# Kernel optimization log

Hardware: AMD Instinct MI355X
Metric: run time of the kernel (lower is better)

## Reference

```python
import jax, jax.numpy as jnp
import numpy as np

T = 0.07
TOPK = 5

def _l2norm(x, axis=-1, eps=1e-12):
    n = jnp.sqrt(jnp.sum(x * x, axis=axis, keepdims=True))
    return x / jnp.maximum(n, eps)

def setup_inputs() -> dict:
    key = jax.random.key(0)
    k1, k2, k3, k4, k5 = jax.random.split(key, 5)
    b, nc, dim, dim_mlp, K = 256, 5, 128, 2048, 65536
    q = jax.random.normal(k1, (b, nc, dim), jnp.float32)
    k = jax.random.normal(k2, (b, dim), jnp.float32)
    q_backbone = jax.random.normal(k3, (b, nc, dim_mlp), jnp.float32)
    # queues are column-normalized buffers, as in __init__
    queue = _l2norm(jax.random.normal(k4, (dim, K), jnp.float32), axis=0)
    queue_backbone = _l2norm(jax.random.normal(k5, (dim_mlp, K), jnp.float32), axis=0)
    return {"q": q, "k": k, "q_backbone": q_backbone,
            "queue": queue, "queue_backbone": queue_backbone}

def reference(q, k, q_backbone, queue, queue_backbone):
    b, nc, dim = q.shape
    dim_mlp = q_backbone.shape[-1]
    qn = _l2norm(q)                 # [b, nc, dim]
    kn = _l2norm(k)                 # [b, dim]
    qb = _l2norm(q_backbone)        # [b, nc, dim_mlp]

    # positive logits: each crop vs its key
    l_pos = jnp.einsum('bnd,bd->bn', qn, kn).reshape(-1, 1)      # [b*nc, 1]
    # negative logits vs queue
    l_neg = jnp.einsum('nc,ck->nk', qn.reshape(-1, dim), queue)  # [b*nc, K]
    logits = jnp.concatenate([l_pos, l_neg], axis=1) / T
    labels = jnp.zeros((logits.shape[0],), dtype=jnp.int32)

    # backbone-space similarities to pick top-k neighbors
    l_neg_backbone = jnp.einsum('nc,ck->nk', qb.reshape(-1, dim_mlp), queue_backbone)

    # pull_topk: softmax CE pulling toward top-k backbone neighbors.
    # scatter-mask + masked mean == gather log-softmax at top-k indices (indices distinct)
    _, knn_idx = jax.lax.top_k(l_neg_backbone, TOPK)             # [b*nc, TOPK]
    log_prob = jax.nn.log_softmax(l_neg / T, axis=1)             # [b*nc, K]
    pos_logp = jnp.take_along_axis(log_prob, knn_idx, axis=1)    # [b*nc, TOPK]
    loss = -jnp.mean(jnp.mean(pos_logp, axis=1))
    return logits, labels, loss
```

## Files before the change

kernel.cpp:

```cpp
#include <hip/hip_runtime.h>
#include <hip/hip_bf16.h>

#define M_     1280
#define DIM    128
#define DMLP   2048
#define KQ     65536
#define NCOLS  65537ull
#define NTOPK  5
#define NCHUNK 256
#define NBLK1  512
#define NTK    32
#define INV_T  14.285714285714286f

typedef __attribute__((ext_vector_type(8))) short bf16x8;
typedef __attribute__((ext_vector_type(4))) float f32x4;

static __device__ __forceinline__ unsigned short f2bf(float x){
  union { __hip_bfloat16 h; unsigned short u; } cv;
  cv.h = __float2bfloat16(x);
  return cv.u;
}

#define GLDS16(gp, lp) __builtin_amdgcn_global_load_lds( \
    (const __attribute__((address_space(1))) void*)(gp), \
    (__attribute__((address_space(3))) void*)(lp), 16, 0, 0)

#define BAR()   asm volatile("s_barrier" ::: "memory")
#define VMW(n)  asm volatile("s_waitcnt vmcnt(" #n ")" ::: "memory")

__global__ __launch_bounds__(256) void transpose_bf16(
    const float* __restrict__ in, unsigned short* __restrict__ out, int R, int C){
  __shared__ float tile[64][65];
  const int c0 = blockIdx.x * 64, r0 = blockIdx.y * 64;
  const int t = threadIdx.x;
  #pragma unroll
  for (int i = 0; i < 4; ++i){
    int lin = t + i * 256;
    int rr = lin >> 4;
    int cc = (lin & 15) * 4;
    const float4 v = *(const float4*)(in + (size_t)(r0 + rr) * C + c0 + cc);
    tile[rr][cc + 0] = v.x; tile[rr][cc + 1] = v.y;
    tile[rr][cc + 2] = v.z; tile[rr][cc + 3] = v.w;
  }
  __syncthreads();
  #pragma unroll
  for (int i = 0; i < 4; ++i){
    int lin = t + i * 256;
    int oc  = lin >> 4;
    int orr = (lin & 15) * 4;
    ushort4 u;
    u.x = f2bf(tile[orr + 0][oc]); u.y = f2bf(tile[orr + 1][oc]);
    u.z = f2bf(tile[orr + 2][oc]); u.w = f2bf(tile[orr + 3][oc]);
    *(ushort4*)(out + (size_t)(c0 + oc) * R + r0 + orr) = u;
  }
}

__global__ __launch_bounds__(128) void normq_kernel(
    const float* __restrict__ q, const float* __restrict__ k,
    unsigned short* __restrict__ qn, float* __restrict__ outp){
  const int i = blockIdx.x;
  const int t = threadIdx.x;
  const float qv = q[(size_t)i * DIM + t];
  const float kv = k[(size_t)(i / 5) * DIM + t];
  float a = qv * qv, b = kv * kv, d = qv * kv;
  #pragma unroll
  for (int s = 32; s >= 1; s >>= 1){
    a += __shfl_down(a, s, 64);
    b += __shfl_down(b, s, 64);
    d += __shfl_down(d, s, 64);
  }
  __shared__ float red[6];
  if ((t & 63) == 0){ red[(t >> 6) * 3 + 0] = a; red[(t >> 6) * 3 + 1] = b; red[(t >> 6) * 3 + 2] = d; }
  __syncthreads();
  const float qq = red[0] + red[3], kk = red[1] + red[4], qk = red[2] + red[5];
  const float qnorm = fmaxf(sqrtf(qq), 1e-12f);
  qn[(size_t)i * DIM + t] = f2bf(qv / qnorm);
  if (t == 0){
    const float knorm = fmaxf(sqrtf(kk), 1e-12f);
    outp[(size_t)i * NCOLS] = (qk / (qnorm * knorm)) * INV_T;
  }
}

__global__ __launch_bounds__(256) void normqb_kernel(
    const float* __restrict__ qb, unsigned short* __restrict__ out){
  const int i = blockIdx.x, t = threadIdx.x;
  const float* p = qb + (size_t)i * DMLP;
  float x[8]; float ss = 0.f;
  #pragma unroll
  for (int j = 0; j < 8; ++j){ x[j] = p[t + j * 256]; ss += x[j] * x[j]; }
  #pragma unroll
  for (int s = 32; s >= 1; s >>= 1) ss += __shfl_down(ss, s, 64);
  __shared__ float r4[4];
  if ((t & 63) == 0) r4[t >> 6] = ss;
  __syncthreads();
  const float tot = r4[0] + r4[1] + r4[2] + r4[3];
  const float inv = 1.0f / fmaxf(sqrtf(tot), 1e-12f);
  unsigned short* o = out + (size_t)i * DMLP;
  #pragma unroll
  for (int j = 0; j < 8; ++j) o[t + j * 256] = f2bf(x[j] * inv);
}

static __device__ __forceinline__ void tk_insert(float* v, int* ix, float nv, int ni){
  if (nv > v[4]){
    v[4] = nv; ix[4] = ni;
    #pragma unroll
    for (int j = 4; j > 0; --j){
      if (v[j] > v[j - 1]){
        float tv = v[j]; v[j] = v[j - 1]; v[j - 1] = tv;
        int   ti = ix[j]; ix[j] = ix[j - 1]; ix[j - 1] = ti;
      }
    }
  }
}

__global__ __launch_bounds__(256) void gemm1_mfma(
    const unsigned short* __restrict__ A, const unsigned short* __restrict__ BT,
    float* __restrict__ outp, float* __restrict__ pm, float* __restrict__ ps){
  __shared__ __attribute__((aligned(16))) unsigned char smem[16512];
  unsigned short* At = (unsigned short*)smem;
  unsigned short* Bt = At + 128 * 32;

  const int t    = threadIdx.x;
  const int lane = t & 63;
  const int wv   = t >> 6;
  const int lid  = lane & 15;
  const int quad = lane >> 4;
  const int m0 = blockIdx.x * 128;
  const int n0 = blockIdx.y * 128;

  f32x4 acc[2][8];
  #pragma unroll
  for (int mt = 0; mt < 2; ++mt)
    #pragma unroll
    for (int nt = 0; nt < 8; ++nt)
      acc[mt][nt] = f32x4{0.f, 0.f, 0.f, 0.f};

  const int arow = t >> 2;
  const int ace  = (t & 3) * 8;

  for (int kt = 0; kt < DIM; kt += 32){
    if (kt) __syncthreads();
    #pragma unroll
    for (int it = 0; it < 2; ++it){
      int row = arow + it * 64;
      GLDS16(A  + (size_t)(m0 + row) * DIM + kt + ace, At + (t + it * 256) * 8);
    }
    #pragma unroll
    for (int it = 0; it < 2; ++it){
      int row = arow + it * 64;
      GLDS16(BT + (size_t)(n0 + row) * DIM + kt + ace, Bt + (t + it * 256) * 8);
    }
    asm volatile("s_waitcnt vmcnt(0)" ::: "memory");
    __syncthreads();

    bf16x8 af[2], bfr[8];
    #pragma unroll
    for (int mt = 0; mt < 2; ++mt)
      af[mt] = *(const bf16x8*)(At + (wv * 32 + mt * 16 + lid) * 32 + quad * 8);
    #pragma unroll
    for (int nt = 0; nt < 8; ++nt)
      bfr[nt] = *(const bf16x8*)(Bt + (nt * 16 + lid) * 32 + quad * 8);
    #pragma unroll
    for (int mt = 0; mt < 2; ++mt)
      #pragma unroll
      for (int nt = 0; nt < 8; ++nt)
        acc[mt][nt] = __builtin_amdgcn_mfma_f32_16x16x32_bf16(af[mt], bfr[nt], acc[mt][nt], 0, 0, 0);
  }

  float mx[2][4], sm[2][4];
  #pragma unroll
  for (int mt = 0; mt < 2; ++mt)
    #pragma unroll
    for (int r = 0; r < 4; ++r) mx[mt][r] = -3.0e38f;
  #pragma unroll
  for (int mt = 0; mt < 2; ++mt)
    #pragma unroll
    for (int nt = 0; nt < 8; ++nt)
      #pragma unroll
      for (int r = 0; r < 4; ++r){
        const int mg = m0 + wv * 32 + mt * 16 + quad * 4 + r;
        const int ng = n0 + nt * 16 + lid;
        const float x = acc[mt][nt][r] * INV_T;
        outp[(size_t)mg * NCOLS + 1 + ng] = x;
        mx[mt][r] = fmaxf(mx[mt][r], x);
      }
  #pragma unroll
  for (int mt = 0; mt < 2; ++mt)
    #pragma unroll
    for (int r = 0; r < 4; ++r){
      #pragma unroll
      for (int s = 8; s >= 1; s >>= 1)
        mx[mt][r] = fmaxf(mx[mt][r], __shfl_xor(mx[mt][r], s, 64));
      sm[mt][r] = 0.f;
    }
  #pragma unroll
  for (int mt = 0; mt < 2; ++mt)
    #pragma unroll
    for (int nt = 0; nt < 8; ++nt)
      #pragma unroll
      for (int r = 0; r < 4; ++r)
        sm[mt][r] += __expf(acc[mt][nt][r] * INV_T - mx[mt][r]);
  #pragma unroll
  for (int mt = 0; mt < 2; ++mt)
    #pragma unroll
    for (int r = 0; r < 4; ++r){
      #pragma unroll
      for (int s = 8; s >= 1; s >>= 1)
        sm[mt][r] += __shfl_xor(sm[mt][r], s, 64);
      if (lid == 0){
        const int mg = m0 + wv * 32 + mt * 16 + quad * 4 + r;
        pm[(size_t)mg * NBLK1 + blockIdx.y] = mx[mt][r];
        ps[(size_t)mg * NBLK1 + blockIdx.y] = sm[mt][r];
      }
    }
}


static __device__ __forceinline__ void stage_half_g2(
    const unsigned short* __restrict__ G, int growbase, int kt,
    unsigned short* dst, int t){
  #pragma unroll
  for (int l = 0; l < 2; ++l){
    const int p = l * 512 + t;
    const int r = p >> 3;
    const int g = (p & 7) ^ (r & 7);
    GLDS16(G + (size_t)(growbase + r) * DMLP + kt * 64 + g * 8, dst + p * 8);
  }
}

#define RDA(mi_, SRC) do { _Pragma("unroll") for (int mf = 0; mf < 4; ++mf){ \
    const int R_ = (mi_) * 128 + wm * 64 + mf * 16 + lid; \
    av[mi_][mf][0] = *(const bf16x8*)((SRC) + R_ * 64 + sw0); \
    av[mi_][mf][1] = *(const bf16x8*)((SRC) + R_ * 64 + sw1); } } while(0)

#define RDB(nj_, SRC) do { _Pragma("unroll") for (int nf = 0; nf < 2; ++nf){ \
    const int S_ = (nj_) * 128 + wn * 32 + nf * 16 + lid; \
    bv[nf][0] = *(const bf16x8*)((SRC) + S_ * 64 + sw0); \
    bv[nf][1] = *(const bf16x8*)((SRC) + S_ * 64 + sw1); } } while(0)

#define MMQ(mi_, nj_) do { __builtin_amdgcn_s_setprio(1); \
    _Pragma("unroll") for (int mf = 0; mf < 4; ++mf) \
    _Pragma("unroll") for (int nf = 0; nf < 2; ++nf){ \
      acc[mi_][nj_][mf][nf] = __builtin_amdgcn_mfma_f32_16x16x32_bf16(av[mi_][mf][0], bv[nf][0], acc[mi_][nj_][mf][nf], 0, 0, 0); \
      acc[mi_][nj_][mf][nf] = __builtin_amdgcn_mfma_f32_16x16x32_bf16(av[mi_][mf][1], bv[nf][1], acc[mi_][nj_][mf][nf], 0, 0, 0); } \
    __builtin_amdgcn_s_setprio(0); } while(0)

__global__ __launch_bounds__(512, 2) void gemm2_topk(
    const unsigned short* __restrict__ A, const unsigned short* __restrict__ BT,
    float* __restrict__ cval, int* __restrict__ cidx){
  __shared__ __attribute__((aligned(16))) unsigned short lds[2][2][256 * 64];

  const int t    = threadIdx.x;
  const int lane = t & 63;
  const int wv   = t >> 6;
  const int wm   = wv >> 2;
  const int wn   = wv & 3;
  const int lid  = lane & 15;
  const int quad = lane >> 4;
  const int l7   = lid & 7;
  const int sw0  = ((quad    ) ^ l7) * 8;
  const int sw1  = ((quad ^ 4) ^ l7) * 8;

  const int h  = blockIdx.x;
  const int wg = (h & 7) * 160 + (h >> 3);
  const int bm = wg % 5;
  const int bn = wg / 5;
  const int m0 = bm * 256;
  const int n0 = bn * 256;

  f32x4 acc[2][2][4][2];
  #pragma unroll
  for (int a = 0; a < 2; ++a)
    #pragma unroll
    for (int b = 0; b < 2; ++b)
      #pragma unroll
      for (int c = 0; c < 4; ++c)
        #pragma unroll
        for (int d = 0; d < 2; ++d)
          acc[a][b][c][d] = f32x4{0.f, 0.f, 0.f, 0.f};

  bf16x8 av[2][4][2];
  bf16x8 bv[2][2];

  stage_half_g2(A,  m0,       0, &lds[0][0][0],        t);
  stage_half_g2(BT, n0,       0, &lds[0][1][0],        t);
  stage_half_g2(A,  m0 + 128, 0, &lds[0][0][128 * 64], t);
  stage_half_g2(BT, n0 + 128, 0, &lds[0][1][128 * 64], t);
  VMW(4);
  BAR();
  RDA(0, &lds[0][0][0]);
  RDB(0, &lds[0][1][0]);

  #pragma unroll 2
  for (int kt = 0; kt < NTK; ++kt){
    unsigned short* curA = &lds[kt & 1][0][0];
    unsigned short* curB = &lds[kt & 1][1][0];
    unsigned short* nxtA = &lds[(kt + 1) & 1][0][0];
    unsigned short* nxtB = &lds[(kt + 1) & 1][1][0];
    const bool pf = (kt + 1 < NTK);

    if (pf) stage_half_g2(A, m0, kt + 1, nxtA, t);
    BAR();
    MMQ(0, 0);
    if (pf){ VMW(4); } else { VMW(2); }
    RDA(1, curA);
    BAR();

    if (pf) stage_half_g2(BT, n0, kt + 1, nxtB, t);
    BAR();
    MMQ(1, 0);
    if (pf){ VMW(4); } else { VMW(0); }
    RDB(1, curB);
    BAR();

    if (pf) stage_half_g2(A, m0 + 128, kt + 1, nxtA + 128 * 64, t);
    BAR();
    MMQ(1, 1);
    BAR();

    if (pf) stage_half_g2(BT, n0 + 128, kt + 1, nxtB + 128 * 64, t);
    BAR();
    MMQ(0, 1);
    if (pf){
      VMW(4);
      RDA(0, nxtA);
      RDB(0, nxtB);
    }
    BAR();
  }

  float* scratch = (float*)&lds[0][0][0];
  const int erow = t >> 2;
  const int eh   = t & 3;
  #pragma unroll
  for (int mi = 0; mi < 2; ++mi){
    float v[5]; int ix[5];
    #pragma unroll
    for (int j = 0; j < 5; ++j){ v[j] = -3.0e38f; ix[j] = 0; }
    #pragma unroll
    for (int nj = 0; nj < 2; ++nj){
      __syncthreads();
      #pragma unroll
      for (int mf = 0; mf < 4; ++mf)
        #pragma unroll
        for (int nf = 0; nf < 2; ++nf)
          #pragma unroll
          for (int r = 0; r < 4; ++r)
            scratch[(wm * 64 + mf * 16 + quad * 4 + r) * 133 + wn * 32 + nf * 16 + lid]
              = acc[mi][nj][mf][nf][r];
      __syncthreads();
      for (int j = 0; j < 32; ++j)
        tk_insert(v, ix, scratch[erow * 133 + j * 4 + eh], n0 + nj * 128 + j * 4 + eh);
    }
    #pragma unroll
    for (int s = 1; s <= 2; s <<= 1){
      float pv[5]; int pi[5];
      #pragma unroll
      for (int j = 0; j < 5; ++j){ pv[j] = __shfl_xor(v[j], s, 64); pi[j] = __shfl_xor(ix[j], s, 64); }
      #pragma unroll
      for (int j = 0; j < 5; ++j) tk_insert(v, ix, pv[j], pi[j]);
    }
    if (eh == 0){
      const int rowg = m0 + mi * 128 + erow;
      const size_t cb = ((size_t)rowg * NCHUNK + bn) * NTOPK;
      #pragma unroll
      for (int j = 0; j < 5; ++j){ cval[cb + j] = v[j]; cidx[cb + j] = ix[j]; }
    }
  }
}

__global__ __launch_bounds__(256) void topk_merge(
    const float* __restrict__ cval, const int* __restrict__ cidx, int* __restrict__ knn){
  const int row = blockIdx.x, t = threadIdx.x;
  float v[5]; int ix[5];
  #pragma unroll
  for (int j = 0; j < 5; ++j){ v[j] = -3.0e38f; ix[j] = 0; }
  const size_t base = (size_t)row * (NCHUNK * NTOPK);
  #pragma unroll
  for (int j = 0; j < 5; ++j){
    const int c = t * 5 + j;
    tk_insert(v, ix, cval[base + c], cidx[base + c]);
  }
  __shared__ float lv[256 * 5];
  __shared__ int   li[256 * 5];
  #pragma unroll
  for (int j = 0; j < 5; ++j){ lv[t * 5 + j] = v[j]; li[t * 5 + j] = ix[j]; }
  __syncthreads();
  if (t < 64){
    float v2[5]; int ix2[5];
    #pragma unroll
    for (int j = 0; j < 5; ++j){ v2[j] = -3.0e38f; ix2[j] = 0; }
    for (int L = 0; L < 4; ++L)
      #pragma unroll
      for (int j = 0; j < 5; ++j)
        tk_insert(v2, ix2, lv[(t * 4 + L) * 5 + j], li[(t * 4 + L) * 5 + j]);
    #pragma unroll
    for (int s = 32; s >= 1; s >>= 1){
      float pv[5]; int pi[5];
      #pragma unroll
      for (int j = 0; j < 5; ++j){ pv[j] = __shfl_down(v2[j], s, 64); pi[j] = __shfl_down(ix2[j], s, 64); }
      #pragma unroll
      for (int j = 0; j < 5; ++j) tk_insert(v2, ix2, pv[j], pi[j]);
    }
    if (t == 0){
      #pragma unroll
      for (int j = 0; j < 5; ++j) knn[(size_t)row * NTOPK + j] = ix2[j];
    }
  }
}

__global__ __launch_bounds__(256) void lse_merge(
    const float* __restrict__ pm, const float* __restrict__ ps,
    float* __restrict__ lse){
  const int row = blockIdx.x, t = threadIdx.x;
  const float* pmr = pm + (size_t)row * NBLK1;
  const float* psr = ps + (size_t)row * NBLK1;
  float m = -1.0e30f, s = 0.f;
  #pragma unroll
  for (int c = 0; c < 2; ++c){
    const float om = pmr[t + c * 256], os = psr[t + c * 256];
    const float nm = fmaxf(m, om);
    s = s * __expf(m - nm) + os * __expf(om - nm);
    m = nm;
  }
  #pragma unroll
  for (int sh = 32; sh >= 1; sh >>= 1){
    const float om = __shfl_down(m, sh, 64), os = __shfl_down(s, sh, 64);
    const float nm = fmaxf(m, om);
    s = s * __expf(m - nm) + os * __expf(om - nm);
    m = nm;
  }
  __shared__ float sm2[4], ss2[4];
  if ((t & 63) == 0){ sm2[t >> 6] = m; ss2[t >> 6] = s; }
  __syncthreads();
  if (t == 0){
    float M = sm2[0], S = ss2[0];
    #pragma unroll
    for (int w = 1; w < 4; ++w){
      const float nm = fmaxf(M, sm2[w]);
      S = S * __expf(M - nm) + ss2[w] * __expf(sm2[w] - nm);
      M = nm;
    }
    lse[row] = M + __logf(S);
  }
}

__global__ __launch_bounds__(256) void loss_kernel(
    const float* __restrict__ logits, const float* __restrict__ lse,
    const int* __restrict__ knn, float* __restrict__ loss){
  const int i = blockIdx.x * 256 + threadIdx.x;
  float c = 0.f;
  if (i < M_){
    const float l = lse[i];
    #pragma unroll
    for (int j = 0; j < 5; ++j){
      const int id = knn[(size_t)i * NTOPK + j];
      c += l - logits[(size_t)i * NCOLS + 1 + id];
    }
    c *= (1.0f / 6400.0f);
  }
  #pragma unroll
  for (int s = 32; s >= 1; s >>= 1) c += __shfl_down(c, s, 64);
  if ((threadIdx.x & 63) == 0) atomicAdd(loss, c);
}

extern "C" void kernel_launch(void* const* d_in, const int* in_sizes, int n_in,
                              void* d_out, int out_size, void* d_ws, size_t ws_size,
                              hipStream_t stream){
  const float* q   = (const float*)d_in[0];
  const float* k   = (const float*)d_in[1];
  const float* qbI = (const float*)d_in[2];
  const float* que = (const float*)d_in[3];
  const float* qbb = (const float*)d_in[4];
  float* out = (float*)d_out;

  unsigned char* w = (unsigned char*)d_ws;
  unsigned short* qn   = (unsigned short*)w; w += (size_t)M_ * DIM  * 2;
  unsigned short* qbn  = (unsigned short*)w; w += (size_t)M_ * DMLP * 2;
  unsigned short* queT = (unsigned short*)w; w += (size_t)KQ * DIM  * 2;
  unsigned short* qbbT = (unsigned short*)w; w += (size_t)KQ * DMLP * 2;
  float* cval = (float*)w;                   w += (size_t)M_ * NCHUNK * NTOPK * 4;
  int*   cidx = (int*)w;                     w += (size_t)M_ * NCHUNK * NTOPK * 4;
  int*   knn  = (int*)w;                     w += (size_t)M_ * NTOPK * 4;
  float* lseb = (float*)w;                   w += (size_t)M_ * 4;
  float* pm   = (float*)w;                   w += (size_t)M_ * NBLK1 * 4;
  float* ps   = (float*)w;                   w += (size_t)M_ * NBLK1 * 4;

  hipMemsetAsync(out + (size_t)M_ * NCOLS, 0, (M_ + 1) * sizeof(float), stream);

  transpose_bf16<<<dim3(KQ / 64, DIM  / 64), 256, 0, stream>>>(que, queT, DIM,  KQ);
  transpose_bf16<<<dim3(KQ / 64, DMLP / 64), 256, 0, stream>>>(qbb, qbbT, DMLP, KQ);
  normq_kernel <<<M_, 128, 0, stream>>>(q, k, qn, out);
  normqb_kernel<<<M_, 256, 0, stream>>>(qbI, qbn);
  gemm1_mfma<<<dim3(10, NBLK1), 256, 0, stream>>>(qn, queT, out, pm, ps);
  gemm2_topk<<<dim3(1280), 512, 0, stream>>>(qbn, qbbT, cval, cidx);
  topk_merge<<<M_, 256, 0, stream>>>(cval, cidx, knn);
  lse_merge<<<M_, 256, 0, stream>>>(pm, ps, lseb);
  loss_kernel<<<(M_ + 255) / 256, 256, 0, stream>>>(out, lseb, knn,
                                                    out + (size_t)M_ * NCOLS + M_);
}
```

Measured before the change: 1.434 ms.

## Deepen GEMM global-to-LDS prefetch to stage half-tiles two k-steps ahead

Restructures the k-loop of the backbone GEMM so the first halves of the A and B tiles for step kt+2 are loaded into the buffer just consumed, while the second halves for kt+1 are loaded during step kt. The last k-step is peeled out of the loop. The aim is to keep more global loads in flight and hide memory latency behind the MFMA work. In exchange the vmcnt wait counts and barrier placement become more intricate, and any reuse of LDS before its reads finish would be a race.

```diff
diff --git a/kernel.cpp b/kernel.cpp
--- a/kernel.cpp
+++ b/kernel.cpp
@@ -286,47 +286,69 @@
   stage_half_g2(BT, n0,       0, &lds[0][1][0],        t);
   stage_half_g2(A,  m0 + 128, 0, &lds[0][0][128 * 64], t);
   stage_half_g2(BT, n0 + 128, 0, &lds[0][1][128 * 64], t);
-  VMW(4);
+  stage_half_g2(A,  m0,       1, &lds[1][0][0],        t);
+  stage_half_g2(BT, n0,       1, &lds[1][1][0],        t);
+  VMW(8);
   BAR();
   RDA(0, &lds[0][0][0]);
   RDB(0, &lds[0][1][0]);
+  BAR();
 
   #pragma unroll 2
-  for (int kt = 0; kt < NTK; ++kt){
+  for (int kt = 0; kt < NTK - 1; ++kt){
     unsigned short* curA = &lds[kt & 1][0][0];
     unsigned short* curB = &lds[kt & 1][1][0];
     unsigned short* nxtA = &lds[(kt + 1) & 1][0][0];
     unsigned short* nxtB = &lds[(kt + 1) & 1][1][0];
-    const bool pf = (kt + 1 < NTK);
-
-    if (pf) stage_half_g2(A, m0, kt + 1, nxtA, t);
+    const bool pf2 = (kt + 2 < NTK);
+
+    VMW(6);
+    stage_half_g2(A, m0 + 128, kt + 1, nxtA + 128 * 64, t);
     BAR();
     MMQ(0, 0);
-    if (pf){ VMW(4); } else { VMW(2); }
     RDA(1, curA);
     BAR();
 
-    if (pf) stage_half_g2(BT, n0, kt + 1, nxtB, t);
+    VMW(6);
+    stage_half_g2(BT, n0 + 128, kt + 1, nxtB + 128 * 64, t);
     BAR();
     MMQ(1, 0);
-    if (pf){ VMW(4); } else { VMW(0); }
     RDB(1, curB);
     BAR();
 
-    if (pf) stage_half_g2(A, m0 + 128, kt + 1, nxtA + 128 * 64, t);
+    if (pf2) stage_half_g2(A, m0, kt + 2, curA, t);
     BAR();
     MMQ(1, 1);
     BAR();
 
-    if (pf) stage_half_g2(BT, n0 + 128, kt + 1, nxtB + 128 * 64, t);
+    if (pf2){
+      VMW(6);
+      stage_half_g2(BT, n0, kt + 2, curB, t);
+    } else {
+      VMW(4);
+    }
     BAR();
     MMQ(0, 1);
-    if (pf){
-      VMW(4);
-      RDA(0, nxtA);
-      RDB(0, nxtB);
-    }
-    BAR();
+    RDA(0, nxtA);
+    RDB(0, nxtB);
+    BAR();
+  }
+
+  {
+    unsigned short* curA = &lds[(NTK - 1) & 1][0][0];
+    unsigned short* curB = &lds[(NTK - 1) & 1][1][0];
+    VMW(2);
+    BAR();
+    MMQ(0, 0);
+    RDA(1, curA);
+    BAR();
+    VMW(0);
+    BAR();
+    MMQ(1, 0);
+    RDB(1, curB);
+    BAR();
+    MMQ(1, 1);
+    MMQ(0, 1);
   }
 
   float* scratch = (float*)&lds[0][0][0];
```

New measurement: 1.447 ms. About the same (+0.9%).

## Restructure gemm2 k-loop to one barrier per tile with deferred MFMA quadrant

Applied to the files above, without the earlier changes.

Rewrites the main loop of the backbone GEMM+top-k kernel. All four next-tile global-to-LDS loads are now issued together, followed by three MFMA quadrants and a single wait plus barrier, replacing eight barriers per k-tile. The fourth quadrant (0,1) is deferred to the start of the next iteration, and once more after the loop, so its LDS reads need no extra sync. Staging addresses are precomputed once per thread. This cuts barrier and wait overhead, but B fragments are now double-buffered in registers, which raises VGPR pressure under the 512x2 launch bound.

```diff
diff --git a/kernel.cpp b/kernel.cpp
--- a/kernel.cpp
+++ b/kernel.cpp
@@ -216,17 +216,7 @@
 }
 
 
-static __device__ __forceinline__ void stage_half_g2(
-    const unsigned short* __restrict__ G, int growbase, int kt,
-    unsigned short* dst, int t){
-  #pragma unroll
-  for (int l = 0; l < 2; ++l){
-    const int p = l * 512 + t;
-    const int r = p >> 3;
-    const int g = (p & 7) ^ (r & 7);
-    GLDS16(G + (size_t)(growbase + r) * DMLP + kt * 64 + g * 8, dst + p * 8);
-  }
-}
+static __device__ __forceinline__ void stage_half_g2_dummy(){}
 
 #define RDA(mi_, SRC) do { _Pragma("unroll") for (int mf = 0; mf < 4; ++mf){ \
     const int R_ = (mi_) * 128 + wm * 64 + mf * 16 + lid; \
@@ -235,15 +225,19 @@
 
 #define RDB(nj_, SRC) do { _Pragma("unroll") for (int nf = 0; nf < 2; ++nf){ \
     const int S_ = (nj_) * 128 + wn * 32 + nf * 16 + lid; \
-    bv[nf][0] = *(const bf16x8*)((SRC) + S_ * 64 + sw0); \
-    bv[nf][1] = *(const bf16x8*)((SRC) + S_ * 64 + sw1); } } while(0)
+    bv[nj_][nf][0] = *(const bf16x8*)((SRC) + S_ * 64 + sw0); \
+    bv[nj_][nf][1] = *(const bf16x8*)((SRC) + S_ * 64 + sw1); } } while(0)
 
 #define MMQ(mi_, nj_) do { __builtin_amdgcn_s_setprio(1); \
     _Pragma("unroll") for (int mf = 0; mf < 4; ++mf) \
     _Pragma("unroll") for (int nf = 0; nf < 2; ++nf){ \
-      acc[mi_][nj_][mf][nf] = __builtin_amdgcn_mfma_f32_16x16x32_bf16(av[mi_][mf][0], bv[nf][0], acc[mi_][nj_][mf][nf], 0, 0, 0); \
-      acc[mi_][nj_][mf][nf] = __builtin_amdgcn_mfma_f32_16x16x32_bf16(av[mi_][mf][1], bv[nf][1], acc[mi_][nj_][mf][nf], 0, 0, 0); } \
+      acc[mi_][nj_][mf][nf] = __builtin_amdgcn_mfma_f32_16x16x32_bf16(av[mi_][mf][0], bv[nj_][nf][0], acc[mi_][nj_][mf][nf], 0, 0, 0); \
+      acc[mi_][nj_][mf][nf] = __builtin_amdgcn_mfma_f32_16x16x32_bf16(av[mi_][mf][1], bv[nj_][nf][1], acc[mi_][nj_][mf][nf], 0, 0, 0); } \
     __builtin_amdgcn_s_setprio(0); } while(0)
+
+#define STAGE(base, kc, dst) do { \
+  GLDS16((base) + ro0 + (kc), (dst) + t * 8); \
+  GLDS16((base) + ro1 + (kc), (dst) + (512 + t) * 8); } while(0)
 
 __global__ __launch_bounds__(512, 2) void gemm2_topk(
     const unsigned short* __restrict__ A, const unsigned short* __restrict__ BT,
@@ -268,6 +262,15 @@
   const int m0 = bm * 256;
   const int n0 = bn * 256;
 
+  const int r0s = t >> 3,        r1s = (512 + t) >> 3;
+  const int g0  = (t & 7) ^ (r0s & 7), g1 = (t & 7) ^ (r1s & 7);
+  const int ro0 = r0s * DMLP + g0 * 8;
+  const int ro1 = r1s * DMLP + g1 * 8;
+  const unsigned short* aB0 = A  + (size_t)m0          * DMLP;
+  const unsigned short* aB1 = A  + (size_t)(m0 + 128)  * DMLP;
+  const unsigned short* bB0 = BT + (size_t)n0          * DMLP;
+  const unsigned short* bB1 = BT + (size_t)(n0 + 128)  * DMLP;
+
   f32x4 acc[2][2][4][2];
   #pragma unroll
   for (int a = 0; a < 2; ++a)
@@ -280,16 +283,14 @@
           acc[a][b][c][d] = f32x4{0.f, 0.f, 0.f, 0.f};
 
   bf16x8 av[2][4][2];
-  bf16x8 bv[2][2];
-
-  stage_half_g2(A,  m0,       0, &lds[0][0][0],        t);
-  stage_half_g2(BT, n0,       0, &lds[0][1][0],        t);
-  stage_half_g2(A,  m0 + 128, 0, &lds[0][0][128 * 64], t);
-  stage_half_g2(BT, n0 + 128, 0, &lds[0][1][128 * 64], t);
-  VMW(4);
+  bf16x8 bv[2][2][2];
+
+  STAGE(aB0, 0, &lds[0][0][0]);
+  STAGE(bB0, 0, &lds[0][1][0]);
+  STAGE(aB1, 0, &lds[0][0][128 * 64]);
+  STAGE(bB1, 0, &lds[0][1][128 * 64]);
+  VMW(0);
   BAR();
-  RDA(0, &lds[0][0][0]);
-  RDB(0, &lds[0][1][0]);
 
   #pragma unroll 2
   for (int kt = 0; kt < NTK; ++kt){
@@ -297,37 +298,30 @@
     unsigned short* curB = &lds[kt & 1][1][0];
     unsigned short* nxtA = &lds[(kt + 1) & 1][0][0];
     unsigned short* nxtB = &lds[(kt + 1) & 1][1][0];
-    const bool pf = (kt + 1 < NTK);
-
-    if (pf) stage_half_g2(A, m0, kt + 1, nxtA, t);
+
+    if (kt) MMQ(0, 1);
+
+    RDA(0, curA);
+    RDB(0, curB);
+
+    if (kt + 1 < NTK){
+      const int kc = (kt + 1) * 64;
+      STAGE(aB0, kc, nxtA);
+      STAGE(bB0, kc, nxtB);
+      STAGE(aB1, kc, nxtA + 128 * 64);
+      STAGE(bB1, kc, nxtB + 128 * 64);
+    }
+
+    MMQ(0, 0);
+    RDA(1, curA);
+    MMQ(1, 0);
+    RDB(1, curB);
+    MMQ(1, 1);
+
+    VMW(0);
     BAR();
-    MMQ(0, 0);
-    if (pf){ VMW(4); } else { VMW(2); }
-    RDA(1, curA);
-    BAR();
-
-    if (pf) stage_half_g2(BT, n0, kt + 1, nxtB, t);
-    BAR();
-    MMQ(1, 0);
-    if (pf){ VMW(4); } else { VMW(0); }
-    RDB(1, curB);
-    BAR();
-
-    if (pf) stage_half_g2(A, m0 + 128, kt + 1, nxtA + 128 * 64, t);
-    BAR();
-    MMQ(1, 1);
-    BAR();
-
-    if (pf) stage_half_g2(BT, n0 + 128, kt + 1, nxtB + 128 * 64, t);
-    BAR();
-    MMQ(0, 1);
-    if (pf){
-      VMW(4);
-      RDA(0, nxtA);
-      RDB(0, nxtB);
-    }
-    BAR();
-  }
+  }
+  MMQ(0, 1);
 
   float* scratch = (float*)&lds[0][0][0];
   const int erow = t >> 2;
```

Result: faster. 1.386 ms (-3.3%).
